# Optimization experiments

Measured on AMD Instinct MI355X. Metric: run time of the kernel, lower is better.

The kernel has to match this reference:

```python
import jax, jax.numpy as jnp
import numpy as np

HEADS = 4
DIM_HEAD = 32
IN_CHANNELS = 256
SCALE = DIM_HEAD ** -0.5
EPS = 1e-5


def setup_inputs() -> dict:
    key = jax.random.key(0)
    ks = jax.random.split(key, 6)
    B, C, H, W = 16, IN_CHANNELS, 64, 64
    inner = HEADS * DIM_HEAD  # 128
    x = jax.random.normal(ks[0], (B, C, H, W), dtype=jnp.float32)
    # 1x1 conv weights are [out_ch, in_ch] (kernel spatial dims are 1)
    w_qkv = jax.random.normal(ks[1], (3 * inner, C), dtype=jnp.float32) * (C ** -0.5)
    w_out = jax.random.normal(ks[2], (C, inner), dtype=jnp.float32) * (inner ** -0.5)
    b_out = jax.random.normal(ks[3], (C,), dtype=jnp.float32) * 0.01
    gn_gamma = jnp.ones((C,), dtype=jnp.float32)
    gn_beta = jnp.zeros((C,), dtype=jnp.float32)
    return {"x": x, "w_qkv": w_qkv, "w_out": w_out, "b_out": b_out,
            "gn_gamma": gn_gamma, "gn_beta": gn_beta}


def reference(x, w_qkv, w_out, b_out, gn_gamma, gn_beta):
    b, c, h, w = x.shape
    n = h * w
    inner = HEADS * DIM_HEAD
    # 1x1 conv (no bias): [b, 3*inner, h, w], then chunk into q,k,v along channels
    qkv = jnp.einsum('oc,bchw->bohw', w_qkv, x)
    qkv = qkv.reshape(b, 3, HEADS, DIM_HEAD, n)  # chunk + 'b (h c) x y -> b h c (x y)'
    q, k, v = qkv[:, 0], qkv[:, 1], qkv[:, 2]    # each [b, heads, dim_head, n]
    q = jax.nn.softmax(q, axis=-2) * SCALE       # softmax over dim_head axis
    k = jax.nn.softmax(k, axis=-1)               # softmax over spatial axis
    context = jnp.einsum('bhdn,bhen->bhde', k, v)  # [b, heads, d, e]
    out = jnp.einsum('bhde,bhdn->bhen', context, q)  # [b, heads, e, n]
    out = out.reshape(b, inner, h, w)            # 'b h c (x y) -> b (h c) x y'
    # out 1x1 conv with bias
    out = jnp.einsum('oc,bchw->bohw', w_out, out) + b_out[None, :, None, None]
    # GroupNorm(num_groups=1): normalize over (C,H,W) per sample, per-channel affine
    mean = jnp.mean(out, axis=(1, 2, 3), keepdims=True)
    var = jnp.var(out, axis=(1, 2, 3), keepdims=True)
    out = (out - mean) * jax.lax.rsqrt(var + EPS)
    return out * gn_gamma[None, :, None, None] + gn_beta[None, :, None, None]
```

## Files before the change

### kernel.cpp

```cpp
#include <hip/hip_runtime.h>
#include <hip/hip_bf16.h>
#include <math.h>

#define B_SZ 16
#define C_IN 256
#define HEADS 4
#define DHEAD 32
#define INNER 128
#define QKV_CH 384
#define N_PIX 4096
#define SCALE_Q 0.17677669529663687f
#define GN_EPS 1e-5f
#define NCHK 64

#define KOFF 16896
#define VOFF 34304

typedef __attribute__((ext_vector_type(8))) short s16x8;
typedef __attribute__((ext_vector_type(4))) float f32x4;
typedef __attribute__((ext_vector_type(8))) unsigned short u16x8;
typedef __attribute__((ext_vector_type(4))) unsigned short u16x4;

#define VMCNT(n) asm volatile("s_waitcnt vmcnt(" #n ")" ::: "memory")
#define LGKMCNT0 asm volatile("s_waitcnt lgkmcnt(0)" ::: "memory")

__device__ __forceinline__ float waveSum(float v) {
#pragma unroll
  for (int off = 32; off > 0; off >>= 1) v += __shfl_down(v, off, 64);
  return v;
}
__device__ __forceinline__ unsigned short f2bf(float f) {
  unsigned int u = __builtin_bit_cast(unsigned int, f);
  unsigned int r = 0x7FFFu + ((u >> 16) & 1u);
  return (unsigned short)((u + r) >> 16);
}
__device__ __forceinline__ float bf2f(unsigned short u) {
  unsigned int x = ((unsigned int)u) << 16;
  return __builtin_bit_cast(float, x);
}

__global__ __launch_bounds__(256) void cvt_w(const float* __restrict__ wq,
                                             const float* __restrict__ wo,
                                             unsigned short* __restrict__ wqb,
                                             unsigned short* __restrict__ wob) {
  const int i = blockIdx.x * 256 + threadIdx.x;
  if (i < QKV_CH * C_IN) wqb[i] = f2bf(wq[i]);
  if (i < C_IN * INNER) wob[i] = f2bf(wo[i]);
}

__global__ __launch_bounds__(512, 4) void qkv_gemm(const unsigned short* __restrict__ A,
                                                   const float* __restrict__ X,
                                                   unsigned short* __restrict__ qsm_t,
                                                   float* __restrict__ ctxp,
                                                   float* __restrict__ mpart,
                                                   float* __restrict__ spart) {
  const int b = blockIdx.y;
  const int n0 = blockIdx.x * 64;
  const int tid = threadIdx.x;
  const int w = tid >> 6, l = tid & 63;
  const int lr = l & 15, kg = l >> 4;
  const int wm = w >> 1, wn = w & 1;

  __shared__ char lds[65536];
  char* As = lds;
  char* Bs = lds + 49152;

  const int c_loc = ((tid >> 3) & 7) + w * 8;
  const int oct = tid & 7;
  const float* xbase = X + (size_t)b * C_IN * N_PIX + (size_t)c_loc * N_PIX + n0 + oct * 8;

  auto ISSUE_A = [&](int kc, int half) {
#pragma unroll
    for (int it = 0; it < 3; ++it) {
      const int idx = it * 512 + tid;
      const int r = idx >> 3;
      const int srcb = ((idx & 7) << 4) ^ ((r & 7) << 4);
      __builtin_amdgcn_global_load_lds(
          (const __attribute__((address_space(1))) void*)((const char*)A +
              ((size_t)(half * 192 + r) * C_IN + kc * 64) * 2 + srcb),
          (__attribute__((address_space(3))) void*)(As + half * 24576 + idx * 16), 16, 0, 0);
    }
  };

  f32x4 xr0, xr1;
  auto ISSUE_X = [&](int kc) {
    const float* xp = xbase + (size_t)(kc * 64) * N_PIX;
    xr0 = *reinterpret_cast<const f32x4*>(xp);
    xr1 = *reinterpret_cast<const f32x4*>(xp + 4);
  };

  auto WRITE_B = [&](int pb) {
#pragma unroll
    for (int j = 0; j < 8; ++j) {
      const int n = oct * 8 + j;
      const float v = (j < 4) ? xr0[j] : xr1[j - 4];
      *reinterpret_cast<unsigned short*>(
          Bs + pb * 8192 + n * 128 + ((2 * c_loc) ^ (((n ^ (n >> 3)) & 7) << 4))) = f2bf(v);
    }
  };

  f32x4 acc[2][3][2] = {};

  auto COMPUTE = [&](int kc, int half) {
    const char* Ab = As + half * 24576;
    const char* Bb = Bs + (kc & 1) * 8192;
#pragma unroll
    for (int ks = 0; ks < 2; ++ks) {
      const int kb = ks * 64 + kg * 16;
      s16x8 av[3], bv[2];
#pragma unroll
      for (int i = 0; i < 3; ++i) {
        const int r = wm * 48 + i * 16 + lr;
        av[i] = *reinterpret_cast<const s16x8*>(Ab + r * 128 + (kb ^ ((r & 7) << 4)));
      }
#pragma unroll
      for (int j = 0; j < 2; ++j) {
        const int n = wn * 32 + j * 16 + lr;
        bv[j] = *reinterpret_cast<const s16x8*>(Bb + n * 128 +
                                                (kb ^ (((n ^ (n >> 3)) & 7) << 4)));
      }
#pragma unroll
      for (int i = 0; i < 3; ++i)
#pragma unroll
        for (int j = 0; j < 2; ++j)
          acc[half][i][j] =
              __builtin_amdgcn_mfma_f32_16x16x32_bf16(av[i], bv[j], acc[half][i][j], 0, 0, 0);
    }
  };

  ISSUE_A(0, 0);
  ISSUE_X(0);
  VMCNT(0);
  WRITE_B(0);
  LGKMCNT0;
  __builtin_amdgcn_s_barrier();

  for (int kc = 0; kc < 4; ++kc) {
    ISSUE_A(kc, 1);
    if (kc < 3) {
      ISSUE_X(kc + 1);
      VMCNT(5);
    } else {
      VMCNT(3);
    }
    __builtin_amdgcn_s_barrier();
    COMPUTE(kc, 0);
    LGKMCNT0;
    __builtin_amdgcn_s_barrier();
    if (kc < 3) {
      ISSUE_A(kc + 1, 0);
      VMCNT(3);
    } else {
      VMCNT(0);
    }
    __builtin_amdgcn_s_barrier();
    if (kc < 3) WRITE_B((kc + 1) & 1);
    COMPUTE(kc, 1);
    LGKMCNT0;
    __builtin_amdgcn_s_barrier();
  }

#pragma unroll
  for (int half = 0; half < 2; ++half)
#pragma unroll
    for (int i = 0; i < 3; ++i)
#pragma unroll
      for (int j = 0; j < 2; ++j) {
        const int chb = half * 192 + wm * 48 + i * 16 + kg * 4;
        const int col = wn * 32 + j * 16 + lr;
        u16x4 pk;
#pragma unroll
        for (int r = 0; r < 4; ++r) pk[r] = f2bf(acc[half][i][j][r]);
        if (chb < 128) {
          *reinterpret_cast<u16x4*>(lds + col * 264 + chb * 2) = pk;
        } else if (chb < 256) {
#pragma unroll
          for (int r = 0; r < 4; ++r)
            *reinterpret_cast<unsigned short*>(lds + KOFF + (chb - 128 + r) * 136 + col * 2) =
                pk[r];
        } else {
#pragma unroll
          for (int r = 0; r < 4; ++r)
            *reinterpret_cast<unsigned short*>(lds + VOFF + (chb - 256 + r) * 136 + col * 2) =
                pk[r];
        }
      }
  LGKMCNT0;
  __builtin_amdgcn_s_barrier();

  if (tid < 256) {
    const int n_loc = tid & 63, h2 = tid >> 6;
    float q[32];
#pragma unroll
    for (int c = 0; c < 8; ++c) {
      u16x4 v4 = *reinterpret_cast<const u16x4*>(lds + n_loc * 264 + h2 * 64 + c * 8);
#pragma unroll
      for (int t = 0; t < 4; ++t) q[c * 4 + t] = bf2f(v4[t]);
    }
    float m = q[0];
#pragma unroll
    for (int t = 1; t < 32; ++t) m = fmaxf(m, q[t]);
    float s = 0.f;
#pragma unroll
    for (int t = 0; t < 32; ++t) {
      q[t] = __expf(q[t] - m);
      s += q[t];
    }
    const float inv = SCALE_Q / s;
    unsigned short* ob = qsm_t + ((size_t)b * N_PIX + n0 + n_loc) * INNER + h2 * DHEAD;
#pragma unroll
    for (int d8 = 0; d8 < 4; ++d8) {
      u16x8 pk;
#pragma unroll
      for (int r = 0; r < 8; ++r) pk[r] = f2bf(q[d8 * 8 + r] * inv);
      *reinterpret_cast<u16x8*>(&ob[d8 * 8]) = pk;
    }
  }

  {
    const int h = w >> 1, et = w & 1;
    float kvv[2][2][8];
#pragma unroll
    for (int dt = 0; dt < 2; ++dt)
#pragma unroll
      for (int ks = 0; ks < 2; ++ks) {
        const char* base = lds + KOFF + (h * 32 + dt * 16 + lr) * 136 + (ks * 32 + kg * 8) * 2;
        u16x4 lo = *reinterpret_cast<const u16x4*>(base);
        u16x4 hi = *reinterpret_cast<const u16x4*>(base + 8);
#pragma unroll
        for (int t = 0; t < 4; ++t) {
          kvv[dt][ks][t] = bf2f(lo[t]);
          kvv[dt][ks][4 + t] = bf2f(hi[t]);
        }
      }
    float m2[2] = {-INFINITY, -INFINITY};
#pragma unroll
    for (int dt = 0; dt < 2; ++dt) {
#pragma unroll
      for (int ks = 0; ks < 2; ++ks)
#pragma unroll
        for (int t = 0; t < 8; ++t) m2[dt] = fmaxf(m2[dt], kvv[dt][ks][t]);
      m2[dt] = fmaxf(m2[dt], __shfl_xor(m2[dt], 16, 64));
      m2[dt] = fmaxf(m2[dt], __shfl_xor(m2[dt], 32, 64));
    }
    float s2[2] = {0.f, 0.f};
    s16x8 ka[2][2];
#pragma unroll
    for (int dt = 0; dt < 2; ++dt) {
#pragma unroll
      for (int ks = 0; ks < 2; ++ks)
#pragma unroll
        for (int t = 0; t < 8; ++t) {
          const float ev = __expf(kvv[dt][ks][t] - m2[dt]);
          s2[dt] += ev;
          ka[dt][ks][t] = (short)f2bf(ev);
        }
      s2[dt] += __shfl_xor(s2[dt], 16, 64);
      s2[dt] += __shfl_xor(s2[dt], 32, 64);
    }
    s16x8 vfrag[2];
#pragma unroll
    for (int ks = 0; ks < 2; ++ks) {
      const char* base = lds + VOFF + (h * 32 + et * 16 + lr) * 136 + (ks * 32 + kg * 8) * 2;
      u16x4 lo = *reinterpret_cast<const u16x4*>(base);
      u16x4 hi = *reinterpret_cast<const u16x4*>(base + 8);
      u16x8 vv;
#pragma unroll
      for (int t = 0; t < 4; ++t) {
        vv[t] = lo[t];
        vv[4 + t] = hi[t];
      }
      vfrag[ks] = __builtin_bit_cast(s16x8, vv);
    }
    f32x4 accc[2] = {};
#pragma unroll
    for (int ks = 0; ks < 2; ++ks)
#pragma unroll
      for (int dt = 0; dt < 2; ++dt)
        accc[dt] = __builtin_amdgcn_mfma_f32_16x16x32_bf16(ka[dt][ks], vfrag[ks], accc[dt], 0, 0, 0);

    const size_t wid = ((size_t)(b * HEADS + h)) * NCHK + blockIdx.x;
    float* cp = ctxp + wid * 1024;
#pragma unroll
    for (int dt = 0; dt < 2; ++dt)
#pragma unroll
      for (int r = 0; r < 4; ++r)
        cp[(dt * 16 + kg * 4 + r) * 32 + et * 16 + lr] = accc[dt][r];
    if (et == 0 && kg == 0) {
      mpart[wid * 32 + lr] = m2[0];
      mpart[wid * 32 + 16 + lr] = m2[1];
      spart[wid * 32 + lr] = s2[0];
      spart[wid * 32 + 16 + lr] = s2[1];
    }
  }
}

__global__ __launch_bounds__(256) void ctx_weff(const float* __restrict__ ctxp,
                                                const float* __restrict__ mpart,
                                                const float* __restrict__ spart,
                                                const unsigned short* __restrict__ wo,
                                                unsigned short* __restrict__ weff) {
  const int bh = blockIdx.x;
  const int b = bh >> 2, h = bh & 3;
  const int tid = threadIdx.x;
  __shared__ float ms[NCHK][32], ss[NCHK][32], fac[NCHK][32];
  __shared__ float inv_l[32];
  __shared__ float cf[1024];
#pragma unroll
  for (int i = 0; i < 8; ++i) {
    const int idx = tid + i * 256;
    ms[idx >> 5][idx & 31] = mpart[(size_t)bh * 2048 + idx];
    ss[idx >> 5][idx & 31] = spart[(size_t)bh * 2048 + idx];
  }
  __syncthreads();
  if (tid < 32) {
    const int d = tid;
    float M = -INFINITY;
#pragma unroll
    for (int c = 0; c < NCHK; ++c) M = fmaxf(M, ms[c][d]);
    float den = 0.f;
#pragma unroll
    for (int c = 0; c < NCHK; ++c) {
      const float f = __expf(ms[c][d] - M);
      fac[c][d] = f;
      den += f * ss[c][d];
    }
    inv_l[d] = 1.0f / den;
  }
  __syncthreads();
  const float* cp = ctxp + (size_t)bh * (NCHK * 1024);
  for (int i = 0; i < 4; ++i) {
    const int idx = tid + i * 256;
    const int d = idx >> 5;
    float a = 0.f;
#pragma unroll
    for (int g = 0; g < 2; ++g) {
      float vals[32];
#pragma unroll
      for (int c = 0; c < 32; ++c) vals[c] = cp[(size_t)(g * 32 + c) * 1024 + idx];
#pragma unroll
      for (int c = 0; c < 32; ++c) a += fac[g * 32 + c][d] * vals[c];
    }
    cf[idx] = a * inv_l[d];
  }
  __syncthreads();

  const int o = tid;
  float wr[32];
  const unsigned short* wp = wo + (size_t)o * INNER + h * DHEAD;
#pragma unroll
  for (int e8 = 0; e8 < 4; ++e8) {
    u16x8 v = *reinterpret_cast<const u16x8*>(wp + e8 * 8);
#pragma unroll
    for (int j = 0; j < 8; ++j) wr[e8 * 8 + j] = bf2f(v[j]);
  }
  unsigned short* op = weff + ((size_t)b * C_IN + o) * INNER + h * DHEAD;
#pragma unroll
  for (int d8 = 0; d8 < 4; ++d8) {
    u16x8 outv;
#pragma unroll
    for (int dd = 0; dd < 8; ++dd) {
      const float* cr = cf + (d8 * 8 + dd) * 32;
      float a = 0.f;
#pragma unroll
      for (int e4 = 0; e4 < 8; ++e4) {
        const f32x4 c4 = *reinterpret_cast<const f32x4*>(cr + e4 * 4);
#pragma unroll
        for (int j = 0; j < 4; ++j) a += wr[e4 * 4 + j] * c4[j];
      }
      outv[dd] = f2bf(a);
    }
    *reinterpret_cast<u16x8*>(op + d8 * 8) = outv;
  }
}

template <bool WRITE>
__global__ __launch_bounds__(256) void out_gemm_t(
    const unsigned short* __restrict__ A, const unsigned short* __restrict__ Bm,
    float* __restrict__ Out, const float* __restrict__ bias,
    float* __restrict__ gn_part, const float* __restrict__ gamma,
    const float* __restrict__ beta) {
  const int id = blockIdx.x;
  const int rank = (id & 7) * 128 + (id >> 3);
  const int b = rank >> 6;
  const int m0 = ((rank >> 5) & 1) * 128;
  const int n0 = (rank & 31) * 128;
  const int tid = threadIdx.x;
  const int w = tid >> 6, l = tid & 63;
  const int lr = l & 15, kg = l >> 4;
  const int mOff = (w >> 1) * 64, nOff = (w & 1) * 64;

  __shared__ unsigned short As[8192];
  __shared__ unsigned short Bs[8192];
  __shared__ float red[8];

  const unsigned short* Ab = A + (size_t)b * C_IN * INNER;
  const unsigned short* Bb = Bm + (size_t)b * N_PIX * INNER;
  f32x4 acc[4][4] = {};

  for (int kc = 0; kc < INNER; kc += 64) {
#pragma unroll
    for (int s = 0; s < 4; ++s) {
      const int blk = (w * 4 + s) * 64 + l;
      const int r = blk >> 3;
      const int c = ((blk & 7) ^ (r & 7)) << 3;
      __builtin_amdgcn_global_load_lds(
          (const __attribute__((address_space(1))) void*)(Ab + (size_t)(m0 + r) * INNER + kc + c),
          (__attribute__((address_space(3))) void*)((char*)As + (w * 4 + s) * 1024), 16, 0, 0);
      __builtin_amdgcn_global_load_lds(
          (const __attribute__((address_space(1))) void*)(Bb + (size_t)(n0 + r) * INNER + kc + c),
          (__attribute__((address_space(3))) void*)((char*)Bs + (w * 4 + s) * 1024), 16, 0, 0);
    }
    __syncthreads();
#pragma unroll
    for (int ks = 0; ks < 2; ++ks) {
      const int kbyte = ks * 64 + kg * 16;
      s16x8 av[4], bv[4];
#pragma unroll
      for (int i = 0; i < 4; ++i) {
        const int row = mOff + i * 16 + lr;
        av[i] = *reinterpret_cast<const s16x8*>(
            (const char*)As + row * 128 + (kbyte ^ ((row & 7) << 4)));
      }
#pragma unroll
      for (int j = 0; j < 4; ++j) {
        const int row = nOff + j * 16 + lr;
        bv[j] = *reinterpret_cast<const s16x8*>(
            (const char*)Bs + row * 128 + (kbyte ^ ((row & 7) << 4)));
      }
#pragma unroll
      for (int i = 0; i < 4; ++i)
#pragma unroll
        for (int j = 0; j < 4; ++j)
          acc[i][j] = __builtin_amdgcn_mfma_f32_16x16x32_bf16(av[i], bv[j], acc[i][j], 0, 0, 0);
    }
    __syncthreads();
  }

  if (!WRITE) {
    float s = 0.f, s2 = 0.f;
#pragma unroll
    for (int i = 0; i < 4; ++i) {
      const int rowb = m0 + mOff + i * 16 + kg * 4;
#pragma unroll
      for (int r = 0; r < 4; ++r) {
        const float bvs = bias[rowb + r];
#pragma unroll
        for (int j = 0; j < 4; ++j) {
          const float v = acc[i][j][r] + bvs;
          s += v;
          s2 += v * v;
        }
      }
    }
    const float S = waveSum(s), S2 = waveSum(s2);
    if (l == 0) {
      red[w] = S;
      red[4 + w] = S2;
    }
    __syncthreads();
    if (tid == 0) {
      gn_part[(size_t)rank * 2 + 0] = red[0] + red[1] + red[2] + red[3];
      gn_part[(size_t)rank * 2 + 1] = red[4] + red[5] + red[6] + red[7];
    }
  } else {
    const int i64 = tid & 63;
    float ps = gn_part[(size_t)(b * 64 + i64) * 2 + 0];
    float ps2 = gn_part[(size_t)(b * 64 + i64) * 2 + 1];
    ps = waveSum(ps);
    ps2 = waveSum(ps2);
    const float invn = 1.0f / (float)(C_IN * N_PIX);
    const float mean = __shfl(ps, 0, 64) * invn;
    const float var = __shfl(ps2, 0, 64) * invn - mean * mean;
    const float istd = rsqrtf(var + GN_EPS);

    float* Ob = Out + (size_t)b * C_IN * N_PIX;
#pragma unroll
    for (int i = 0; i < 4; ++i) {
      const int rowb = m0 + mOff + i * 16 + kg * 4;
#pragma unroll
      for (int r = 0; r < 4; ++r) {
        const int ch = rowb + r;
        const float bvs = bias[ch];
        const float g = gamma[ch] * istd;
        const float be = beta[ch];
#pragma unroll
        for (int j = 0; j < 4; ++j) {
          const int col = n0 + nOff + j * 16 + lr;
          const float v = acc[i][j][r] + bvs;
          Ob[(size_t)ch * N_PIX + col] = (v - mean) * g + be;
        }
      }
    }
  }
}

extern "C" void kernel_launch(void* const* d_in, const int* in_sizes, int n_in,
                              void* d_out, int out_size, void* d_ws, size_t ws_size,
                              hipStream_t stream) {
  const float* x = (const float*)d_in[0];
  const float* w_qkv = (const float*)d_in[1];
  const float* w_out = (const float*)d_in[2];
  const float* b_out = (const float*)d_in[3];
  const float* gamma = (const float*)d_in[4];
  const float* beta = (const float*)d_in[5];
  float* out = (float*)d_out;

  char* p = (char*)d_ws;
  unsigned short* qsm_t = (unsigned short*)p; p += (size_t)B_SZ * N_PIX * INNER * 2;
  unsigned short* wq_bf = (unsigned short*)p; p += (size_t)QKV_CH * C_IN * 2;
  unsigned short* wo_bf = (unsigned short*)p; p += (size_t)C_IN * INNER * 2;
  float* ctxp = (float*)p;    p += (size_t)B_SZ * HEADS * NCHK * 1024 * 4;
  float* mpart = (float*)p;   p += (size_t)B_SZ * HEADS * NCHK * 32 * 4;
  float* spart = (float*)p;   p += (size_t)B_SZ * HEADS * NCHK * 32 * 4;
  unsigned short* weff = (unsigned short*)p; p += (size_t)B_SZ * C_IN * INNER * 2;
  float* gn_part = (float*)p; p += (size_t)1024 * 2 * 4;

  cvt_w<<<dim3(384), 256, 0, stream>>>(w_qkv, w_out, wq_bf, wo_bf);
  qkv_gemm<<<dim3(64, B_SZ), 512, 0, stream>>>(wq_bf, x, qsm_t, ctxp, mpart, spart);
  ctx_weff<<<dim3(64), 256, 0, stream>>>(ctxp, mpart, spart, wo_bf, weff);
  out_gemm_t<false><<<dim3(1024), 256, 0, stream>>>(
      weff, qsm_t, nullptr, b_out, gn_part, nullptr, nullptr);
  out_gemm_t<true><<<dim3(1024), 256, 0, stream>>>(
      weff, qsm_t, out, b_out, gn_part, gamma, beta);
}
```

Baseline: 79.88 us.

## Compute GroupNorm statistics via Gram matrices instead of a second GEMM pass

Replaces the stats-only output GEMM pass with an algebraic computation: the Gram matrix Q·Qᵀ and the column sums of Q are accumulated per batch with atomics. A small kernel then combines them with Weffᵀ·Weff and the bias terms to get the mean and variance. The final GEMM then writes the normalized output in a single pass. This removes a full recomputation of the output GEMM, at the cost of two extra low-occupancy kernels, atomics, and potential cancellation error in the variance.

```diff
diff --git a/kernel.cpp b/kernel.cpp
--- a/kernel.cpp
+++ b/kernel.cpp
@@ -42,10 +42,14 @@
 __global__ __launch_bounds__(256) void cvt_w(const float* __restrict__ wq,
                                              const float* __restrict__ wo,
                                              unsigned short* __restrict__ wqb,
-                                             unsigned short* __restrict__ wob) {
+                                             unsigned short* __restrict__ wob,
+                                             float* __restrict__ gq,
+                                             float* __restrict__ qsb) {
   const int i = blockIdx.x * 256 + threadIdx.x;
   if (i < QKV_CH * C_IN) wqb[i] = f2bf(wq[i]);
   if (i < C_IN * INNER) wob[i] = f2bf(wo[i]);
+  for (int j = i; j < 16 * 16384; j += 384 * 256) gq[j] = 0.f;
+  if (i < 16 * 128) qsb[i] = 0.f;
 }
 
 __global__ __launch_bounds__(512, 4) void qkv_gemm(const unsigned short* __restrict__ A,
@@ -295,6 +299,83 @@
   }
 }
 
+__global__ __launch_bounds__(256, 4) void gq_gram(const unsigned short* __restrict__ qsm,
+                                                  float* __restrict__ gq,
+                                                  float* __restrict__ qsb) {
+  const int ns = blockIdx.x;
+  const int b = blockIdx.y;
+  const int tid = threadIdx.x;
+  const int w = tid >> 6, l = tid & 63;
+  const int lr = l & 15, kg = l >> 4;
+  const int qr = w >> 1, qc = w & 1;
+
+  __shared__ unsigned short T[64 * 128];
+
+  const unsigned short* qb = qsm + ((size_t)b * N_PIX + ns * 512) * INNER;
+
+  f32x4 acc[4][4] = {};
+  for (int tile = 0; tile < 8; ++tile) {
+    {
+      const int nr = tid >> 2, kseg = (tid & 3) * 32;
+      const unsigned short* src = qb + (size_t)(tile * 64 + nr) * INNER + kseg;
+#pragma unroll
+      for (int s = 0; s < 4; ++s)
+        *reinterpret_cast<u16x8*>(&T[nr * 128 + kseg + s * 8]) =
+            *reinterpret_cast<const u16x8*>(src + s * 8);
+    }
+    __syncthreads();
+#pragma unroll
+    for (int ks = 0; ks < 2; ++ks) {
+      s16x8 af[4], bf[4];
+#pragma unroll
+      for (int i = 0; i < 4; ++i) {
+        u16x8 tmp;
+#pragma unroll
+        for (int t = 0; t < 8; ++t)
+          tmp[t] = T[(ks * 32 + kg * 8 + t) * 128 + qr * 64 + i * 16 + lr];
+        af[i] = __builtin_bit_cast(s16x8, tmp);
+      }
+#pragma unroll
+      for (int j = 0; j < 4; ++j) {
+        u16x8 tmp;
+#pragma unroll
+        for (int t = 0; t < 8; ++t)
+          tmp[t] = T[(ks * 32 + kg * 8 + t) * 128 + qc * 64 + j * 16 + lr];
+        bf[j] = __builtin_bit_cast(s16x8, tmp);
+      }
+#pragma unroll
+      for (int i = 0; i < 4; ++i)
+#pragma unroll
+        for (int j = 0; j < 4; ++j)
+          acc[i][j] = __builtin_amdgcn_mfma_f32_16x16x32_bf16(af[i], bf[j], acc[i][j], 0, 0, 0);
+    }
+    __syncthreads();
+  }
+  float* gqb = gq + (size_t)b * 16384;
+#pragma unroll
+  for (int i = 0; i < 4; ++i)
+#pragma unroll
+    for (int j = 0; j < 4; ++j)
+#pragma unroll
+      for (int r = 0; r < 4; ++r) {
+        const int k = qr * 64 + i * 16 + kg * 4 + r;
+        const int k2 = qc * 64 + j * 16 + lr;
+        atomicAdd(&gqb[k * 128 + k2], acc[i][j][r]);
+      }
+  {
+    const int k = tid & 127, half = tid >> 7;
+    const unsigned short* src = qsm + ((size_t)b * N_PIX + ns * 512 + half * 256) * INNER + k;
+    float s = 0.f;
+    for (int n0 = 0; n0 < 256; n0 += 16) {
+      float t = 0.f;
+#pragma unroll
+      for (int n = 0; n < 16; ++n) t += bf2f(src[(size_t)(n0 + n) * INNER]);
+      s += t;
+    }
+    atomicAdd(&qsb[b * 128 + k], s);
+  }
+}
+
 __global__ __launch_bounds__(256) void ctx_weff(const float* __restrict__ ctxp,
                                                 const float* __restrict__ mpart,
                                                 const float* __restrict__ spart,
@@ -374,11 +455,125 @@
   }
 }
 
-template <bool WRITE>
-__global__ __launch_bounds__(256) void out_gemm_t(
+__global__ __launch_bounds__(256, 4) void gn_stats(const unsigned short* __restrict__ weff,
+                                                   const float* __restrict__ gq,
+                                                   const float* __restrict__ qsb,
+                                                   const float* __restrict__ bias,
+                                                   float* __restrict__ gnstat) {
+  const int b = blockIdx.x;
+  const int tid = threadIdx.x;
+  const int w = tid >> 6, l = tid & 63;
+  const int lr = l & 15, kg = l >> 4;
+  const int qr = w >> 1, qc = w & 1;
+
+  __shared__ unsigned short T[64 * 128];
+  __shared__ float red[20];
+
+  const unsigned short* wb = weff + (size_t)b * C_IN * INNER;
+
+  f32x4 acc[4][4] = {};
+  for (int tile = 0; tile < 4; ++tile) {
+    {
+      const int cr = tid >> 2, kseg = (tid & 3) * 32;
+      const unsigned short* src = wb + (size_t)(tile * 64 + cr) * INNER + kseg;
+#pragma unroll
+      for (int s = 0; s < 4; ++s)
+        *reinterpret_cast<u16x8*>(&T[cr * 128 + kseg + s * 8]) =
+            *reinterpret_cast<const u16x8*>(src + s * 8);
+    }
+    __syncthreads();
+#pragma unroll
+    for (int ks = 0; ks < 2; ++ks) {
+      s16x8 af[4], bf[4];
+#pragma unroll
+      for (int i = 0; i < 4; ++i) {
+        u16x8 tmp;
+#pragma unroll
+        for (int t = 0; t < 8; ++t)
+          tmp[t] = T[(ks * 32 + kg * 8 + t) * 128 + qr * 64 + i * 16 + lr];
+        af[i] = __builtin_bit_cast(s16x8, tmp);
+      }
+#pragma unroll
+      for (int j = 0; j < 4; ++j) {
+        u16x8 tmp;
+#pragma unroll
+        for (int t = 0; t < 8; ++t)
+          tmp[t] = T[(ks * 32 + kg * 8 + t) * 128 + qc * 64 + j * 16 + lr];
+        bf[j] = __builtin_bit_cast(s16x8, tmp);
+      }
+#pragma unroll
+      for (int i = 0; i < 4; ++i)
+#pragma unroll
+        for (int j = 0; j < 4; ++j)
+          acc[i][j] = __builtin_amdgcn_mfma_f32_16x16x32_bf16(af[i], bf[j], acc[i][j], 0, 0, 0);
+    }
+    __syncthreads();
+  }
+  const float* gqb = gq + (size_t)b * 16384;
+  float s2y = 0.f;
+#pragma unroll
+  for (int i = 0; i < 4; ++i)
+#pragma unroll
+    for (int j = 0; j < 4; ++j)
+#pragma unroll
+      for (int r = 0; r < 4; ++r) {
+        const int k = qr * 64 + i * 16 + kg * 4 + r;
+        const int k2 = qc * 64 + j * 16 + lr;
+        s2y += acc[i][j][r] * gqb[k * 128 + k2];
+      }
+  s2y = waveSum(s2y);
+  if (l == 0) red[w] = s2y;
+
+  float pc = 0.f, pb2 = 0.f;
+  if (tid < 128) {
+    const int k = tid;
+    float wcs = 0.f, wbs = 0.f;
+    for (int ch0 = 0; ch0 < 256; ch0 += 16) {
+#pragma unroll
+      for (int c = 0; c < 16; ++c) {
+        const float wv = bf2f(wb[(size_t)(ch0 + c) * INNER + k]);
+        wcs += wv;
+        wbs += bias[ch0 + c] * wv;
+      }
+    }
+    const float qs = qsb[b * 128 + k];
+    pc = wcs * qs;
+    pb2 = wbs * qs;
+  }
+  pc = waveSum(pc);
+  pb2 = waveSum(pb2);
+  if (l == 0 && w < 2) {
+    red[4 + w] = pc;
+    red[6 + w] = pb2;
+  }
+  const float bv = bias[tid];
+  float b1 = waveSum(bv);
+  float b2 = waveSum(bv * bv);
+  if (l == 0) {
+    red[8 + w] = b1;
+    red[12 + w] = b2;
+  }
+  __syncthreads();
+  if (tid == 0) {
+    const float S2y = red[0] + red[1] + red[2] + red[3];
+    const float S1y = red[4] + red[5];
+    const float CR = red[6] + red[7];
+    const float Sb1 = red[8] + red[9] + red[10] + red[11];
+    const float Sb2 = red[12] + red[13] + red[14] + red[15];
+    const float S1 = S1y + 4096.f * Sb1;
+    const float S2 = S2y + 2.f * CR + 4096.f * Sb2;
+    const float invn = 1.0f / (float)(C_IN * N_PIX);
+    const float mean = S1 * invn;
+    const float var = S2 * invn - mean * mean;
+    gnstat[b * 2 + 0] = mean;
+    gnstat[b * 2 + 1] = rsqrtf(var + GN_EPS);
+  }
+}
+
+__global__ __launch_bounds__(256) void out_apply(
     const unsigned short* __restrict__ A, const unsigned short* __restrict__ Bm,
     float* __restrict__ Out, const float* __restrict__ bias,
-    float* __restrict__ gn_part, const float* __restrict__ gamma,
+    const float* __restrict__ gnstat, const float* __restrict__ gamma,
     const float* __restrict__ beta) {
   const int id = blockIdx.x;
   const int rank = (id & 7) * 128 + (id >> 3);
@@ -392,7 +587,6 @@
 
   __shared__ unsigned short As[8192];
   __shared__ unsigned short Bs[8192];
-  __shared__ float red[8];
 
   const unsigned short* Ab = A + (size_t)b * C_IN * INNER;
   const unsigned short* Bb = Bm + (size_t)b * N_PIX * INNER;
@@ -437,59 +631,24 @@
     __syncthreads();
   }
 
-  if (!WRITE) {
-    float s = 0.f, s2 = 0.f;
-#pragma unroll
-    for (int i = 0; i < 4; ++i) {
-      const int rowb = m0 + mOff + i * 16 + kg * 4;
-#pragma unroll
-      for (int r = 0; r < 4; ++r) {
-        const float bvs = bias[rowb + r];
-#pragma unroll
-        for (int j = 0; j < 4; ++j) {
-          const float v = acc[i][j][r] + bvs;
-          s += v;
-          s2 += v * v;
-        }
-      }
-    }
-    const float S = waveSum(s), S2 = waveSum(s2);
-    if (l == 0) {
-      red[w] = S;
-      red[4 + w] = S2;
-    }
-    __syncthreads();
-    if (tid == 0) {
-      gn_part[(size_t)rank * 2 + 0] = red[0] + red[1] + red[2] + red[3];
-      gn_part[(size_t)rank * 2 + 1] = red[4] + red[5] + red[6] + red[7];
-    }
-  } else {
-    const int i64 = tid & 63;
-    float ps = gn_part[(size_t)(b * 64 + i64) * 2 + 0];
-    float ps2 = gn_part[(size_t)(b * 64 + i64) * 2 + 1];
-    ps = waveSum(ps);
-    ps2 = waveSum(ps2);
-    const float invn = 1.0f / (float)(C_IN * N_PIX);
-    const float mean = __shfl(ps, 0, 64) * invn;
-    const float var = __shfl(ps2, 0, 64) * invn - mean * mean;
-    const float istd = rsqrtf(var + GN_EPS);
-
-    float* Ob = Out + (size_t)b * C_IN * N_PIX;
-#pragma unroll
-    for (int i = 0; i < 4; ++i) {
-      const int rowb = m0 + mOff + i * 16 + kg * 4;
-#pragma unroll
-      for (int r = 0; r < 4; ++r) {
-        const int ch = rowb + r;
-        const float bvs = bias[ch];
-        const float g = gamma[ch] * istd;
-        const float be = beta[ch];
-#pragma unroll
-        for (int j = 0; j < 4; ++j) {
-          const int col = n0 + nOff + j * 16 + lr;
-          const float v = acc[i][j][r] + bvs;
-          Ob[(size_t)ch * N_PIX + col] = (v - mean) * g + be;
-        }
+  const float mean = gnstat[b * 2 + 0];
+  const float istd = gnstat[b * 2 + 1];
+
+  float* Ob = Out + (size_t)b * C_IN * N_PIX;
+#pragma unroll
+  for (int i = 0; i < 4; ++i) {
+    const int rowb = m0 + mOff + i * 16 + kg * 4;
+#pragma unroll
+    for (int r = 0; r < 4; ++r) {
+      const int ch = rowb + r;
+      const float bvs = bias[ch];
+      const float g = gamma[ch] * istd;
+      const float be = beta[ch];
+#pragma unroll
+      for (int j = 0; j < 4; ++j) {
+        const int col = n0 + nOff + j * 16 + lr;
+        const float v = acc[i][j][r] + bvs;
+        Ob[(size_t)ch * N_PIX + col] = (v - mean) * g + be;
       }
     }
   }
@@ -514,13 +673,15 @@
   float* mpart = (float*)p;   p += (size_t)B_SZ * HEADS * NCHK * 32 * 4;
   float* spart = (float*)p;   p += (size_t)B_SZ * HEADS * NCHK * 32 * 4;
   unsigned short* weff = (unsigned short*)p; p += (size_t)B_SZ * C_IN * INNER * 2;
-  float* gn_part = (float*)p; p += (size_t)1024 * 2 * 4;
-
-  cvt_w<<<dim3(384), 256, 0, stream>>>(w_qkv, w_out, wq_bf, wo_bf);
+  float* gq = (float*)p;      p += (size_t)B_SZ * 16384 * 4;
+  float* qsb = (float*)p;     p += (size_t)B_SZ * 128 * 4;
+  float* gnstat = (float*)p;  p += 128;
+
+  cvt_w<<<dim3(384), 256, 0, stream>>>(w_qkv, w_out, wq_bf, wo_bf, gq, qsb);
   qkv_gemm<<<dim3(64, B_SZ), 512, 0, stream>>>(wq_bf, x, qsm_t, ctxp, mpart, spart);
+  gq_gram<<<dim3(8, B_SZ), 256, 0, stream>>>(qsm_t, gq, qsb);
   ctx_weff<<<dim3(64), 256, 0, stream>>>(ctxp, mpart, spart, wo_bf, weff);
-  out_gemm_t<false><<<dim3(1024), 256, 0, stream>>>(
-      weff, qsm_t, nullptr, b_out, gn_part, nullptr, nullptr);
-  out_gemm_t<true><<<dim3(1024), 256, 0, stream>>>(
-      weff, qsm_t, out, b_out, gn_part, gamma, beta);
-}
+  gn_stats<<<dim3(B_SZ), 256, 0, stream>>>(weff, gq, qsb, b_out, gnstat);
+  out_apply<<<dim3(1024), 256, 0, stream>>>(
+      weff, qsm_t, out, b_out, gnstat, gamma, beta);
+}
```

After: 112.0 us. 1.4x slower.
